# Performance work log

Hardware: AMD Instinct MI355X
Metric: run time of the kernel (lower is better)

Reference implementation:

```python
import jax, jax.numpy as jnp
import numpy as np

N = 100000      # nodes
E = 1600000     # directed edges (before self loops)
F_IN = 3        # node_feature_dim
H = 32          # hidden_dim
BN_EPS = 1e-5


def _linear_params(k, fan_in, fan_out):
    lim = 1.0 / np.sqrt(fan_in)
    kw, kb = jax.random.split(k)
    W = jax.random.uniform(kw, (fan_in, fan_out), jnp.float32, -lim, lim)
    b = jax.random.uniform(kb, (fan_out,), jnp.float32, -lim, lim)
    return W, b


def setup_inputs() -> dict:
    key = jax.random.key(0)
    ks = jax.random.split(key, 12)
    x = jax.random.normal(ks[0], (N, F_IN), jnp.float32)
    edge_index = jax.random.randint(ks[1], (2, E), 0, N, dtype=jnp.int64)
    node_type = jax.random.randint(ks[2], (N,), 0, 3, dtype=jnp.int64)
    W1, b1 = _linear_params(ks[3], F_IN, H)
    W2, b2 = _linear_params(ks[4], H, H)
    W3, b3 = _linear_params(ks[5], H, H)
    g1 = jnp.ones((H,), jnp.float32); be1 = jnp.zeros((H,), jnp.float32)
    g2 = jnp.ones((H,), jnp.float32); be2 = jnp.zeros((H,), jnp.float32)
    Wc1, bc1 = _linear_params(ks[6], H, H // 2)
    Wc2, bc2 = _linear_params(ks[7], H // 2, 1)
    Wd1, bd1 = _linear_params(ks[8], H, H // 2)
    Wd2, bd2 = _linear_params(ks[9], H // 2, 1)
    return dict(x=x, edge_index=edge_index, node_type=node_type,
                W1=W1, b1=b1, W2=W2, b2=b2, W3=W3, b3=b3,
                g1=g1, be1=be1, g2=g2, be2=be2,
                Wc1=Wc1, bc1=bc1, Wc2=Wc2, bc2=bc2,
                Wd1=Wd1, bd1=bd1, Wd2=Wd2, bd2=bd2)


def reference(x, edge_index, node_type, W1, b1, W2, b2, W3, b3,
              g1, be1, g2, be2, Wc1, bc1, Wc2, bc2, Wd1, bd1, Wd2, bd2):
    n = x.shape[0]
    # GCNConv (PyG default): add self loops, symmetric deg^-1/2 normalization
    loop = jnp.arange(n, dtype=edge_index.dtype)
    src = jnp.concatenate([edge_index[0], loop])  # [E+N]
    dst = jnp.concatenate([edge_index[1], loop])
    deg = jax.ops.segment_sum(jnp.ones_like(dst, dtype=x.dtype), dst, num_segments=n)
    dinv = jnp.where(deg > 0, jax.lax.rsqrt(jnp.maximum(deg, 1.0)), 0.0)
    norm = dinv[src] * dinv[dst]  # [E+N]

    def conv(h, W, b):
        msg = (h @ W)[src] * norm[:, None]                  # gather + scale
        return jax.ops.segment_sum(msg, dst, num_segments=n) + b  # scatter-add

    def bn(h, g, be):  # BatchNorm1d with batch statistics (training math)
        mu = h.mean(axis=0)
        var = ((h - mu) ** 2).mean(axis=0)
        return (h - mu) * jax.lax.rsqrt(var + BN_EPS) * g + be

    h = bn(jax.nn.relu(conv(x, W1, b1)), g1, be1)   # dropout = identity (eval)
    h = bn(jax.nn.relu(conv(h, W2, b2)), g2, be2)
    h = jax.nn.relu(conv(h, W3, b3))

    cand_mask = node_type == 0
    cand_emb = h[cand_mask]                                 # [C, H]
    cand_scores = (jax.nn.relu(cand_emb @ Wc1 + bc1) @ Wc2 + bc2)[:, 0]

    w = jax.nn.softmax(h.sum(axis=1))[:, None]              # [N,1] importance
    g_emb = (h * w).sum(axis=0, keepdims=True)              # [1, H]
    dn = (jax.nn.relu(g_emb @ Wd1 + bd1) @ Wd2 + bd2).reshape(())

    logits = jnp.concatenate([cand_scores, dn[None]], axis=0)
    cand_idx = jnp.nonzero(cand_mask)[0]
    return logits, cand_idx
```

## Files before the change

kernel.cpp:

```cpp
#include <hip/hip_runtime.h>

typedef unsigned int uint;
typedef unsigned char uchar;

#define NB_MAX 256
#define NPB_MAX 2048

#if defined(__has_builtin)
#if __has_builtin(__builtin_amdgcn_cvt_pk_f32_fp8) && __has_builtin(__builtin_amdgcn_cvt_pk_fp8_f32)
#define HW_FP8 1
#endif
#endif

typedef __attribute__((ext_vector_type(2))) float v2f;

static __device__ __forceinline__ uint f2fp8_sw(float v) {
    v = fminf(fmaxf(v, -448.f), 448.f);
    uint u = __float_as_uint(v);
    uint s = (u >> 24) & 0x80u;
    uint mag = u & 0x7FFFFFFFu;
    uint r = mag + 0x7FFFFu + ((mag >> 20) & 1u);
    if (r < 0x3C800000u) return s;
    uint e8 = (r - 0x3C000000u) >> 20;
    return s | min(e8, 0x7Eu);
}
static __device__ __forceinline__ float fp82f(uint b) {
    uint mag = b & 0x7Fu;
    uint bits = ((b & 0x80u) << 24) | ((mag << 20) + 0x3C000000u);
    return mag ? __uint_as_float(bits) : 0.f;
}
static __device__ __forceinline__ void dec8(uint2 v, float* o) {
#ifdef HW_FP8
    v2f a = __builtin_amdgcn_cvt_pk_f32_fp8((int)v.x, false);
    v2f b = __builtin_amdgcn_cvt_pk_f32_fp8((int)v.x, true);
    v2f c = __builtin_amdgcn_cvt_pk_f32_fp8((int)v.y, false);
    v2f d = __builtin_amdgcn_cvt_pk_f32_fp8((int)v.y, true);
    o[0]=a.x; o[1]=a.y; o[2]=b.x; o[3]=b.y;
    o[4]=c.x; o[5]=c.y; o[6]=d.x; o[7]=d.y;
#else
    o[0]=fp82f(v.x&0xFF); o[1]=fp82f((v.x>>8)&0xFF); o[2]=fp82f((v.x>>16)&0xFF); o[3]=fp82f(v.x>>24);
    o[4]=fp82f(v.y&0xFF); o[5]=fp82f((v.y>>8)&0xFF); o[6]=fp82f((v.y>>16)&0xFF); o[7]=fp82f(v.y>>24);
#endif
}
static __device__ __forceinline__ uint2 enc8(const float* o) {
#ifdef HW_FP8
    int rx = __builtin_amdgcn_cvt_pk_fp8_f32(o[0], o[1], 0, false);
    rx = __builtin_amdgcn_cvt_pk_fp8_f32(o[2], o[3], rx, true);
    int ry = __builtin_amdgcn_cvt_pk_fp8_f32(o[4], o[5], 0, false);
    ry = __builtin_amdgcn_cvt_pk_fp8_f32(o[6], o[7], ry, true);
    return make_uint2((uint)rx, (uint)ry);
#else
    uint2 r;
    r.x = f2fp8_sw(o[0]) | (f2fp8_sw(o[1])<<8) | (f2fp8_sw(o[2])<<16) | (f2fp8_sw(o[3])<<24);
    r.y = f2fp8_sw(o[4]) | (f2fp8_sw(o[5])<<8) | (f2fp8_sw(o[6])<<16) | (f2fp8_sw(o[7])<<24);
    return r;
#endif
}
static __device__ __forceinline__ void dec32(const uchar* row, float* o) {
    const uint4* r4 = (const uint4*)row;
    uint4 A = r4[0], B = r4[1];
    dec8(make_uint2(A.x,A.y), o); dec8(make_uint2(A.z,A.w), o+8);
    dec8(make_uint2(B.x,B.y), o+16); dec8(make_uint2(B.z,B.w), o+24);
}
static __device__ __forceinline__ void enc32(const float* o, uchar* row) {
    uint2 a = enc8(o), b = enc8(o+8), c = enc8(o+16), d = enc8(o+24);
    uint4* r4 = (uint4*)row;
    r4[0] = make_uint4(a.x,a.y,b.x,b.y);
    r4[1] = make_uint4(c.x,c.y,d.x,d.y);
}

static __device__ __forceinline__ unsigned wave_incl_scan(unsigned v) {
    int lane = threadIdx.x & 63;
    #pragma unroll
    for (int d = 1; d < 64; d <<= 1) {
        unsigned t = (unsigned)__shfl_up((int)v, d, 64);
        if (lane >= d) v += t;
    }
    return v;
}

static __device__ void block_excl_scan(const uint* in, uint* out, int n, uint* wscr) {
    int tid = threadIdx.x;
    int lane = tid & 63, wid = tid >> 6;
    int base = tid * 8;
    uint v[8], pre[8], s = 0;
    #pragma unroll
    for (int k = 0; k < 8; k++) v[k] = (base + k < n) ? in[base + k] : 0u;
    #pragma unroll
    for (int k = 0; k < 8; k++) { pre[k] = s; s += v[k]; }
    uint is = wave_incl_scan(s);
    __syncthreads();
    if (lane == 63) wscr[wid] = is;
    __syncthreads();
    uint woff = 0;
    for (int wI = 0; wI < wid; wI++) woff += wscr[wI];
    uint excl = is - s + woff;
    #pragma unroll
    for (int k = 0; k < 8; k++) if (base + k < n) out[base + k] = excl + pre[k];
    __syncthreads();
}

__global__ __launch_bounds__(256) void bucket_hist_kernel(const int* src, const int* dst,
                                                          const int* nt, uint* bcnt, uint* bcand,
                                                          int E, int N, int NB, int shift) {
    __shared__ uint bh[NB_MAX], ch[NB_MAX];
    int tid = threadIdx.x;
    bh[tid] = 0; ch[tid] = 0;
    __syncthreads();
    int gs = gridDim.x * 256;
    for (int i = blockIdx.x * 256 + tid; i < E; i += gs) {
        int d = dst[i], s = src[i];
        if ((uint)d < (uint)N && (uint)s < (uint)N) atomicAdd(&bh[d >> shift], 1u);
    }
    for (int i = blockIdx.x * 256 + tid; i < N; i += gs) {
        if (nt[i] == 0) atomicAdd(&ch[i >> shift], 1u);
    }
    __syncthreads();
    if (bh[tid]) atomicAdd(&bcnt[tid], bh[tid]);
    if (ch[tid]) atomicAdd(&bcand[tid], ch[tid]);
}

__global__ __launch_bounds__(256) void partition_kernel(const int* src, const int* dst,
                                                        const uint* bcnt, uint* alloc0,
                                                        uint* staging, int E, int N, int shift) {
    __shared__ uint bbase_s[NB_MAX];
    __shared__ uint lh[NB_MAX], gb[NB_MAX];
    __shared__ uint ws4[4];
    int tid = threadIdx.x;
    int lane = tid & 63, wid = tid >> 6;
    uint a = bcnt[tid];
    uint ia = wave_incl_scan(a);
    if (lane == 63) ws4[wid] = ia;
    __syncthreads();
    uint off = 0;
    for (int wI = 0; wI < wid; wI++) off += ws4[wI];
    bbase_s[tid] = ia - a + off;
    lh[tid] = 0;
    __syncthreads();
    int base = blockIdx.x * 2048;
    uint mask = (1u << shift) - 1u;
    int breg[8];
    uint rreg[8], pk8[8];
    #pragma unroll
    for (int k = 0; k < 8; k++) {
        int e = base + k * 256 + tid;
        breg[k] = -1;
        if (e < E) {
            int s = src[e], d = dst[e];
            if ((uint)d < (uint)N && (uint)s < (uint)N) {
                int b = d >> shift;
                pk8[k] = (((uint)d & mask) << 17) | (uint)s;
                breg[k] = b;
                rreg[k] = atomicAdd(&lh[b], 1u);
            }
        }
    }
    __syncthreads();
    gb[tid] = lh[tid] ? (bbase_s[tid] + atomicAdd(&alloc0[tid], lh[tid])) : 0u;
    __syncthreads();
    #pragma unroll
    for (int k = 0; k < 8; k++) {
        if (breg[k] >= 0)
            staging[gb[breg[k]] + rreg[k]] = pk8[k];
    }
}

__global__ __launch_bounds__(256) void local_csr_kernel(const uint* staging, const uint* bcnt,
                                                        const uint* bcand, const int* nt,
                                                        const float* x,
                                                        int* csr_src, uint* csr_off, uint* cand_pos,
                                                        float* dinv, float4* xs,
                                                        int N, int shift, int NB) {
    __shared__ uint deg[NPB_MAX];
    __shared__ uint ofs[NPB_MAX];
    __shared__ uint ws4[4];
    __shared__ uint sb[4];
    int b = blockIdx.x, tid = threadIdx.x;
    int lane = tid & 63, wid = tid >> 6;
    uint a = bcnt[tid];
    uint ia = wave_incl_scan(a);
    if (lane == 63) ws4[wid] = ia;
    __syncthreads();
    uint off = 0;
    for (int wI = 0; wI < wid; wI++) off += ws4[wI];
    if (tid == b) { sb[0] = ia - a + off; sb[1] = ia + off; }
    __syncthreads();
    uint c = bcand[tid];
    uint ic = wave_incl_scan(c);
    if (lane == 63) ws4[wid] = ic;
    __syncthreads();
    uint offc = 0;
    for (int wI = 0; wI < wid; wI++) offc += ws4[wI];
    if (tid == b) sb[2] = ic - c + offc;
    __syncthreads();
    uint ebase = sb[0], eend = sb[1], cb = sb[2];
    int nbase = b << shift;
    int ncount = min(1 << shift, N - nbase);
    for (int i = tid; i < ncount; i += 256) deg[i] = 0;
    __syncthreads();
    for (uint p = ebase + tid; p < eend; p += 256)
        atomicAdd(&deg[staging[p] >> 17], 1u);
    __syncthreads();
    block_excl_scan(deg, ofs, ncount, ws4);
    for (int i = tid; i < ncount; i += 256)
        csr_off[nbase + i] = ebase + ofs[i];
    if (b == NB - 1 && tid == 0) csr_off[N] = eend;
    for (int i = tid; i < ncount; i += 256) {
        int g = nbase + i;
        float di = rsqrtf((float)(deg[i] + 1u));
        dinv[g] = di;
        xs[g] = make_float4(x[3*g] * di, x[3*g+1] * di, x[3*g+2] * di, 0.f);
    }
    __syncthreads();
    for (int i = tid; i < ncount; i += 256) deg[i] = 0;
    __syncthreads();
    for (uint p = ebase + tid; p < eend; p += 256) {
        uint pkv = staging[p];
        uint dl = pkv >> 17;
        uint pos = ebase + ofs[dl] + atomicAdd(&deg[dl], 1u);
        csr_src[pos] = (int)(pkv & 0x1FFFFu);
    }
    __syncthreads();
    for (int i = tid; i < ncount; i += 256) deg[i] = (nt[nbase + i] == 0) ? 1u : 0u;
    __syncthreads();
    block_excl_scan(deg, ofs, ncount, ws4);
    for (int i = tid; i < ncount; i += 256) cand_pos[nbase + i] = cb + ofs[i];
}

__global__ __launch_bounds__(256) void agg1_kernel(const float* xs, const int* csr_src,
                                                   const uint* csr_off, const float* dinv,
                                                   const float* W1, const float* b1, uchar* hb,
                                                   int n, float* stats_sum, float* stats_sq,
                                                   uint* gt) {
    const int tid = threadIdx.x;
    const int wave = tid >> 6;
    const int lane = tid & 63;
    const int c4 = lane & 3;
    const int slot = lane >> 2;
    const int qlead = lane & ~3;
    __shared__ float W1s[96];
    __shared__ uint s_lt, s_chunk;
    if (tid < 96) W1s[tid] = W1[tid];
    float bv[8];
    #pragma unroll
    for (int j = 0; j < 8; j++) bv[j] = b1[c4 * 8 + j];
    float bs[8], bq[8];
    #pragma unroll
    for (int j = 0; j < 8; j++) { bs[j] = 0.f; bq[j] = 0.f; }
    __syncthreads();
    while (true) {
        if (tid == 0) s_chunk = atomicAdd(gt, 1u);
        __syncthreads();
        uint cbase = s_chunk * 128u;
        if (cbase >= (uint)n) break;
        uint avail = min((uint)n - cbase, 128u);
        if (tid == 0) s_lt = 0u;
        __syncthreads();
        while (true) {
            uint li = 0;
            if (c4 == 0) li = atomicAdd(&s_lt, 1u);
            li = (uint)__shfl((int)li, qlead, 64);
            if (li >= avail) break;
            uint node = cbase + li;
            uint s = csr_off[node], e = csr_off[node + 1];
            float acc = xs[(size_t)node * 4 + c4];
            for (uint p = s; p < e; p += 8) {
                uint idx[8];
                float wg[8];
                #pragma unroll
                for (int j = 0; j < 8; j++) {
                    uint q = p + (uint)j;
                    uint qc = min(q, e - 1u);
                    idx[j] = (uint)csr_src[qc];
                    wg[j] = (q < e) ? 1.f : 0.f;
                }
                #pragma unroll
                for (int j = 0; j < 8; j++)
                    acc = fmaf(wg[j], xs[(size_t)idx[j] * 4 + c4], acc);
            }
            float u = dinv[node] * acc;
            float u0 = __shfl(u, qlead, 64);
            float u1 = __shfl(u, qlead + 1, 64);
            float u2 = __shfl(u, qlead + 2, 64);
            float hv[8];
            #pragma unroll
            for (int j = 0; j < 8; j++) {
                int ch = c4 * 8 + j;
                float o = u0 * W1s[ch] + u1 * W1s[32 + ch] + u2 * W1s[64 + ch] + bv[j];
                hv[j] = fmaxf(o, 0.f);
            }
            *(uint2*)(hb + (size_t)node * 32 + c4 * 8) = enc8(hv);
            #pragma unroll
            for (int j = 0; j < 8; j++) { bs[j] += hv[j]; bq[j] += hv[j] * hv[j]; }
        }
        __syncthreads();
    }
    #pragma unroll
    for (int m = 4; m < 64; m <<= 1) {
        #pragma unroll
        for (int j = 0; j < 8; j++) {
            bs[j] += __shfl_xor(bs[j], m, 64);
            bq[j] += __shfl_xor(bq[j], m, 64);
        }
    }
    __shared__ float ssum[4][32], ssq[4][32];
    if (slot == 0) {
        #pragma unroll
        for (int j = 0; j < 8; j++) { ssum[wave][c4 * 8 + j] = bs[j]; ssq[wave][c4 * 8 + j] = bq[j]; }
    }
    __syncthreads();
    if (tid < 32) {
        atomicAdd(&stats_sum[tid], ssum[0][tid] + ssum[1][tid] + ssum[2][tid] + ssum[3][tid]);
        atomicAdd(&stats_sq[tid],  ssq[0][tid] + ssq[1][tid] + ssq[2][tid] + ssq[3][tid]);
    }
}

__global__ __launch_bounds__(256) void gemmf_kernel(const uchar* hb, const float* stats_sum,
                                                    const float* stats_sq, const float* g,
                                                    const float* be, const float* W,
                                                    const float* dinv, uchar* zb, int n,
                                                    float inv_n) {
    __shared__ float Ws[1024];
    __shared__ float cs[32];
    __shared__ float a_s[32], d_s[32];
    int tid = threadIdx.x;
    if (tid < 32) {
        float mu = stats_sum[tid] * inv_n;
        float var = fmaxf(stats_sq[tid] * inv_n - mu * mu, 0.f);
        float a = g[tid] * rsqrtf(var + 1e-5f);
        a_s[tid] = a;
        d_s[tid] = be[tid] - mu * a;
    }
    __syncthreads();
    #pragma unroll
    for (int t = tid; t < 1024; t += 256) Ws[t] = a_s[t >> 5] * W[t];
    if (tid < 32) {
        float c = 0.f;
        for (int k = 0; k < 32; k++) c += d_s[k] * W[k * 32 + tid];
        cs[tid] = c;
    }
    __syncthreads();
    int i = blockIdx.x * 256 + tid;
    if (i >= n) return;
    float hk[32], acc[32];
    dec32(hb + (size_t)i * 32, hk);
    #pragma unroll
    for (int j = 0; j < 32; j++) acc[j] = cs[j];
    #pragma unroll
    for (int k = 0; k < 32; k++) {
        float h0 = hk[k];
        #pragma unroll
        for (int j = 0; j < 32; j++) acc[j] += h0 * Ws[k * 32 + j];
    }
    float di = dinv[i];
    #pragma unroll
    for (int j = 0; j < 32; j++) acc[j] *= di;
    enc32(acc, zb + (size_t)i * 32);
}

template<int MODE>
__global__ __launch_bounds__(256) void agg_kernel(const uchar* zb, const int* csr_src,
                                                  const uint* csr_off, const float* dinv,
                                                  const float* bias, uchar* hb, int n,
                                                  float* stats_sum, float* stats_sq,
                                                  float* rowsum, uint* maxkey, uint* gt) {
    const int tid = threadIdx.x;
    const int wave = tid >> 6;
    const int lane = tid & 63;
    const int c4 = lane & 3;
    const int slot = lane >> 2;
    const int qlead = lane & ~3;
    __shared__ uint s_lt, s_chunk;
    float bv[8];
    #pragma unroll
    for (int j = 0; j < 8; j++) bv[j] = bias[c4 * 8 + j];
    float bs[8], bq[8];
    if (MODE == 0) {
        #pragma unroll
        for (int j = 0; j < 8; j++) { bs[j] = 0.f; bq[j] = 0.f; }
    }
    float lmax = -3.0e38f;
    while (true) {
        if (tid == 0) s_chunk = atomicAdd(gt, 1u);
        __syncthreads();
        uint cbase = s_chunk * 128u;
        if (cbase >= (uint)n) break;
        uint avail = min((uint)n - cbase, 128u);
        if (tid == 0) s_lt = 0u;
        __syncthreads();
        while (true) {
            uint li = 0;
            if (c4 == 0) li = atomicAdd(&s_lt, 1u);
            li = (uint)__shfl((int)li, qlead, 64);
            if (li >= avail) break;
            uint node = cbase + li;
            uint s = csr_off[node], e = csr_off[node + 1];
            float acc[8];
            dec8(*(const uint2*)(zb + (size_t)node * 32 + c4 * 8), acc);
            for (uint p = s; p < e; p += 8) {
                uint idx[8];
                float wg[8];
                #pragma unroll
                for (int j = 0; j < 8; j++) {
                    uint q = p + (uint)j;
                    uint qc = min(q, e - 1u);
                    idx[j] = (uint)csr_src[qc];
                    wg[j] = (q < e) ? 1.f : 0.f;
                }
                #pragma unroll
                for (int j = 0; j < 8; j++) {
                    float t[8];
                    dec8(*(const uint2*)(zb + (size_t)idx[j] * 32 + c4 * 8), t);
                    #pragma unroll
                    for (int cI = 0; cI < 8; cI++) acc[cI] = fmaf(wg[j], t[cI], acc[cI]);
                }
            }
            float di = dinv[node];
            float hv[8];
            #pragma unroll
            for (int j = 0; j < 8; j++) hv[j] = fmaxf(di * acc[j] + bv[j], 0.f);
            *(uint2*)(hb + (size_t)node * 32 + c4 * 8) = enc8(hv);
            if (MODE == 0) {
                #pragma unroll
                for (int j = 0; j < 8; j++) { bs[j] += hv[j]; bq[j] += hv[j] * hv[j]; }
            } else {
                float rs = ((hv[0] + hv[1]) + (hv[2] + hv[3])) + ((hv[4] + hv[5]) + (hv[6] + hv[7]));
                rs += __shfl_xor(rs, 1, 64);
                rs += __shfl_xor(rs, 2, 64);
                if (c4 == 0) { rowsum[node] = rs; lmax = fmaxf(lmax, rs); }
            }
        }
        __syncthreads();
    }
    if (MODE == 0) {
        #pragma unroll
        for (int m = 4; m < 64; m <<= 1) {
            #pragma unroll
            for (int j = 0; j < 8; j++) {
                bs[j] += __shfl_xor(bs[j], m, 64);
                bq[j] += __shfl_xor(bq[j], m, 64);
            }
        }
        __shared__ float ssum[4][32], ssq[4][32];
        if (slot == 0) {
            #pragma unroll
            for (int j = 0; j < 8; j++) { ssum[wave][c4 * 8 + j] = bs[j]; ssq[wave][c4 * 8 + j] = bq[j]; }
        }
        __syncthreads();
        if (tid < 32) {
            atomicAdd(&stats_sum[tid], ssum[0][tid] + ssum[1][tid] + ssum[2][tid] + ssum[3][tid]);
            atomicAdd(&stats_sq[tid],  ssq[0][tid] + ssq[1][tid] + ssq[2][tid] + ssq[3][tid]);
        }
    } else {
        #pragma unroll
        for (int m = 1; m < 64; m <<= 1) lmax = fmaxf(lmax, __shfl_xor(lmax, m, 64));
        __shared__ float lm[4];
        if (lane == 0) lm[wave] = lmax;
        __syncthreads();
        if (tid == 0) {
            float m = fmaxf(fmaxf(lm[0], lm[1]), fmaxf(lm[2], lm[3]));
            uint u = __float_as_uint(m);
            uint key = (u & 0x80000000u) ? ~u : (u | 0x80000000u);
            atomicMax(maxkey, key);
        }
    }
}

__global__ __launch_bounds__(256) void head_kernel(const uchar* hb, const int* nt,
                                                   const uint* pos, const float* Wc1,
                                                   const float* bc1, const float* Wc2,
                                                   const float* bc2, const float* rowsum,
                                                   const uint* maxkey, float* gvec, float* Zp,
                                                   uint* ticket, const float* Wd1,
                                                   const float* bd1, const float* Wd2,
                                                   const float* bd2, float* out, int n, int C) {
    __shared__ float W1s[512], b1s[16], W2s[16];
    __shared__ float ls[256];
    __shared__ float ge[32], tt[16];
    __shared__ int lastflag;
    int tid = threadIdx.x;
    for (int t = tid; t < 512; t += 256) W1s[t] = Wc1[t];
    if (tid < 16) { b1s[tid] = bc1[tid]; W2s[tid] = Wc2[tid]; }
    __syncthreads();
    int i = blockIdx.x * 256 + tid;
    if (i < n && nt[i] == 0) {
        float hv[32];
        dec32(hb + (size_t)i * 32, hv);
        float s = bc2[0];
        #pragma unroll
        for (int j = 0; j < 16; j++) {
            float u = b1s[j];
            #pragma unroll
            for (int k = 0; k < 32; k++) u += hv[k] * W1s[k * 16 + j];
            s += fmaxf(u, 0.f) * W2s[j];
        }
        s = fminf(fmaxf(s, -1000.f), 1000.f);
        uint p = pos[i];
        if (p < (uint)C) {
            out[p] = s;
            out[C + 1 + p] = (float)i;
        }
    }
    uint key = *maxkey;
    float M = 0.f;
    if (key != 0u) M = (key & 0x80000000u) ? __uint_as_float(key ^ 0x80000000u) : __uint_as_float(~key);
    int lane = tid & 31, grp = tid >> 5;
    int stride = gridDim.x * 8;
    float accZ = 0.f, accg = 0.f;
    for (int node = blockIdx.x * 8 + grp; node < n; node += stride) {
        float ew = __expf(rowsum[node] - M);
        accg += fp82f(hb[(size_t)node * 32 + lane]) * ew;
        if (lane == 0) accZ += ew;
    }
    ls[tid] = accg;
    __syncthreads();
    if (tid < 32) {
        float a = 0.f;
        #pragma unroll
        for (int g = 0; g < 8; g++) a += ls[tid + 32 * g];
        atomicAdd(&gvec[tid], a);
    }
    __syncthreads();
    ls[tid] = (lane == 0) ? accZ : 0.f;
    __syncthreads();
    if (tid == 0) {
        float a = 0.f;
        for (int t = 0; t < 256; t += 32) a += ls[t];
        atomicAdd(Zp, a);
        __threadfence();
        uint old = atomicAdd(ticket, 1u);
        lastflag = (old == gridDim.x - 1) ? 1 : 0;
    }
    __syncthreads();
    if (lastflag) {
        __threadfence();
        if (tid < 32) ge[tid] = atomicAdd(&gvec[tid], 0.f);
        if (tid == 0) ls[0] = atomicAdd(Zp, 0.f);
        __syncthreads();
        float Zv = fmaxf(ls[0], 1e-30f);
        if (tid < 32) ge[tid] /= Zv;
        __syncthreads();
        if (tid < 16) {
            float s = bd1[tid];
            for (int k = 0; k < 32; k++) s += ge[k] * Wd1[k * 16 + tid];
            tt[tid] = fmaxf(s, 0.f);
        }
        __syncthreads();
        if (tid == 0) {
            float s = bd2[0];
            for (int j = 0; j < 16; j++) s += tt[j] * Wd2[j];
            out[C] = fminf(fmaxf(s, -1000.f), 1000.f);
        }
    }
}

extern "C" void kernel_launch(void* const* d_in, const int* in_sizes, int n_in,
                              void* d_out, int out_size, void* d_ws, size_t ws_size,
                              hipStream_t stream) {
    const float* x   = (const float*)d_in[0];
    const int*   ei  = (const int*)d_in[1];
    const int*   nt  = (const int*)d_in[2];
    const float* W1  = (const float*)d_in[3];  const float* b1  = (const float*)d_in[4];
    const float* W2  = (const float*)d_in[5];  const float* b2  = (const float*)d_in[6];
    const float* W3  = (const float*)d_in[7];  const float* b3  = (const float*)d_in[8];
    const float* g1  = (const float*)d_in[9];  const float* be1 = (const float*)d_in[10];
    const float* g2  = (const float*)d_in[11]; const float* be2 = (const float*)d_in[12];
    const float* Wc1 = (const float*)d_in[13]; const float* bc1 = (const float*)d_in[14];
    const float* Wc2 = (const float*)d_in[15]; const float* bc2 = (const float*)d_in[16];
    const float* Wd1 = (const float*)d_in[17]; const float* bd1 = (const float*)d_in[18];
    const float* Wd2 = (const float*)d_in[19]; const float* bd2 = (const float*)d_in[20];

    const int N = in_sizes[0] / 3;
    const int E = in_sizes[1] / 2;
    const int C = (out_size - 1) / 2;
    const int* e_src = ei;
    const int* e_dst = ei + E;
    float* out = (float*)d_out;

    int shift = 9;
    while (((N + (1 << shift) - 1) >> shift) > NB_MAX) shift++;
    const int NB = (N + (1 << shift) - 1) >> shift;

    char* w = (char*)d_ws;
    auto alloc = [&](size_t bytes) { void* p = (void*)w; w += (bytes + 255) & ~(size_t)255; return p; };
    float*    stats  = (float*)alloc(256 * 4);
    uint*     bcnt   = (uint*)alloc(NB_MAX * 4);
    uint*     bcand  = (uint*)alloc(NB_MAX * 4);
    uint*     alloc0 = (uint*)alloc(NB_MAX * 4);
    size_t zero_bytes = (size_t)((char*)w - (char*)stats);
    float*    dinv   = (float*)alloc((size_t)N * 4);
    uint*     csr_off= (uint*)alloc((size_t)(N + 1) * 4);
    uint*     cand_pos=(uint*)alloc((size_t)N * 4);
    float*    rowsum = (float*)alloc((size_t)N * 4);
    int*      csr_src= (int*)alloc((size_t)E * 4);
    uint*     staging= (uint*)alloc((size_t)E * 4);
    uchar*    zb     = (uchar*)alloc((size_t)N * 32);
    uchar*    hb     = (uchar*)alloc((size_t)N * 32);
    float4*   xs     = (float4*)zb;

    float* sum1 = stats;       float* sq1 = stats + 32;
    float* sum2 = stats + 64;  float* sq2 = stats + 96;
    float* gvec = stats + 128; float* Zp  = stats + 160;
    uint* maxkey = (uint*)(stats + 161);
    uint* ticket = (uint*)(stats + 162);
    uint* gt1 = (uint*)(stats + 163);
    uint* gt2 = (uint*)(stats + 164);
    uint* gt3 = (uint*)(stats + 165);

    hipMemsetAsync(stats, 0, zero_bytes, stream);

    const int gN   = (N + 255) / 256;
    const int gPar = (E + 2047) / 2048;
    int gAgg = (N + 127) / 128;
    if (gAgg > 512) gAgg = 512;
    const float inv_n = 1.0f / (float)N;

    hipLaunchKernelGGL(bucket_hist_kernel, dim3(784), dim3(256), 0, stream, e_src, e_dst, nt, bcnt, bcand, E, N, NB, shift);
    hipLaunchKernelGGL(partition_kernel, dim3(gPar), dim3(256), 0, stream, e_src, e_dst, bcnt, alloc0, staging, E, N, shift);
    hipLaunchKernelGGL(local_csr_kernel, dim3(NB), dim3(256), 0, stream, staging, bcnt, bcand, nt,
                       x, csr_src, csr_off, cand_pos, dinv, xs, N, shift, NB);

    hipLaunchKernelGGL(agg1_kernel, dim3(gAgg), dim3(256), 0, stream, (const float*)xs, csr_src, csr_off,
                       dinv, W1, b1, hb, N, sum1, sq1, gt1);

    hipLaunchKernelGGL(gemmf_kernel, dim3(gN), dim3(256), 0, stream, hb, sum1, sq1, g1, be1, W2, dinv, zb, N, inv_n);
    hipLaunchKernelGGL((agg_kernel<0>), dim3(gAgg), dim3(256), 0, stream, zb, csr_src, csr_off,
                       dinv, b2, hb, N, sum2, sq2, rowsum, maxkey, gt2);

    hipLaunchKernelGGL(gemmf_kernel, dim3(gN), dim3(256), 0, stream, hb, sum2, sq2, g2, be2, W3, dinv, zb, N, inv_n);
    hipLaunchKernelGGL((agg_kernel<1>), dim3(gAgg), dim3(256), 0, stream, zb, csr_src, csr_off,
                       dinv, b3, hb, N, sum1, sq1, rowsum, maxkey, gt3);

    hipLaunchKernelGGL(head_kernel, dim3(gN), dim3(256), 0, stream, hb, nt, cand_pos,
                       Wc1, bc1, Wc2, bc2, rowsum, maxkey, gvec, Zp, ticket,
                       Wd1, bd1, Wd2, bd2, out, N, C);
}
```

Measured before the change: 319.0 us.

## Replace block-level chunk scheduling with per-wave global atomic work stealing

The aggregation kernels used to take a 128-node chunk per block through a global atomic, then hand nodes to lane quads through an LDS atomic, with block barriers around each chunk. Now each wave takes 16 nodes at once from the global counter and gives one node to each quad, so the barriers and the LDS atomics are gone. The grid grows to 1024 blocks. The trade is more global atomic traffic, coarser per-wave balancing, and idle quads when a wave's nodes have uneven degrees.

```diff
diff --git a/kernel.cpp b/kernel.cpp
--- a/kernel.cpp
+++ b/kernel.cpp
@@ -239,7 +239,6 @@
     const int slot = lane >> 2;
     const int qlead = lane & ~3;
     __shared__ float W1s[96];
-    __shared__ uint s_lt, s_chunk;
     if (tid < 96) W1s[tid] = W1[tid];
     float bv[8];
     #pragma unroll
@@ -249,19 +248,12 @@
     for (int j = 0; j < 8; j++) { bs[j] = 0.f; bq[j] = 0.f; }
     __syncthreads();
     while (true) {
-        if (tid == 0) s_chunk = atomicAdd(gt, 1u);
-        __syncthreads();
-        uint cbase = s_chunk * 128u;
-        if (cbase >= (uint)n) break;
-        uint avail = min((uint)n - cbase, 128u);
-        if (tid == 0) s_lt = 0u;
-        __syncthreads();
-        while (true) {
-            uint li = 0;
-            if (c4 == 0) li = atomicAdd(&s_lt, 1u);
-            li = (uint)__shfl((int)li, qlead, 64);
-            if (li >= avail) break;
-            uint node = cbase + li;
+        uint base = 0;
+        if (lane == 0) base = atomicAdd(gt, 16u);
+        base = (uint)__shfl((int)base, 0, 64);
+        if (base >= (uint)n) break;
+        uint node = base + (uint)slot;
+        if (node < (uint)n) {
             uint s = csr_off[node], e = csr_off[node + 1];
             float acc = xs[(size_t)node * 4 + c4];
             for (uint p = s; p < e; p += 8) {
@@ -293,7 +285,6 @@
             #pragma unroll
             for (int j = 0; j < 8; j++) { bs[j] += hv[j]; bq[j] += hv[j] * hv[j]; }
         }
-        __syncthreads();
     }
     #pragma unroll
     for (int m = 4; m < 64; m <<= 1) {
@@ -369,8 +360,6 @@
     const int lane = tid & 63;
     const int c4 = lane & 3;
     const int slot = lane >> 2;
-    const int qlead = lane & ~3;
-    __shared__ uint s_lt, s_chunk;
     float bv[8];
     #pragma unroll
     for (int j = 0; j < 8; j++) bv[j] = bias[c4 * 8 + j];
@@ -381,19 +370,12 @@
     }
     float lmax = -3.0e38f;
     while (true) {
-        if (tid == 0) s_chunk = atomicAdd(gt, 1u);
-        __syncthreads();
-        uint cbase = s_chunk * 128u;
-        if (cbase >= (uint)n) break;
-        uint avail = min((uint)n - cbase, 128u);
-        if (tid == 0) s_lt = 0u;
-        __syncthreads();
-        while (true) {
-            uint li = 0;
-            if (c4 == 0) li = atomicAdd(&s_lt, 1u);
-            li = (uint)__shfl((int)li, qlead, 64);
-            if (li >= avail) break;
-            uint node = cbase + li;
+        uint base = 0;
+        if (lane == 0) base = atomicAdd(gt, 16u);
+        base = (uint)__shfl((int)base, 0, 64);
+        if (base >= (uint)n) break;
+        uint node = base + (uint)slot;
+        if (node < (uint)n) {
             uint s = csr_off[node], e = csr_off[node + 1];
             float acc[8];
             dec8(*(const uint2*)(zb + (size_t)node * 32 + c4 * 8), acc);
@@ -430,7 +412,6 @@
                 if (c4 == 0) { rowsum[node] = rs; lmax = fmaxf(lmax, rs); }
             }
         }
-        __syncthreads();
     }
     if (MODE == 0) {
         #pragma unroll
@@ -611,8 +592,7 @@
 
     const int gN   = (N + 255) / 256;
     const int gPar = (E + 2047) / 2048;
-    int gAgg = (N + 127) / 128;
-    if (gAgg > 512) gAgg = 512;
+    int gAgg = 1024;
     const float inv_n = 1.0f / (float)N;
 
     hipLaunchKernelGGL(bucket_hist_kernel, dim3(784), dim3(256), 0, stream, e_src, e_dst, nt, bcnt, bcand, E, N, NB, shift);
```

Result: slower. 610.1 us (+91.3%).
